# Kernel optimization log

Measured on AMD Instinct MI355X. Metric: run time of the kernel, lower is better.

Reference implementation:

```python
import jax, jax.numpy as jnp
import numpy as np

N_NODES = 100000
N_EDGES = 800000
D_R = 128   # node feature dim
D_H = 96    # edge message dim
D_OUT = 96  # output Linear out_features (bias removed per remove_bias)


def setup_inputs() -> dict:
    key = jax.random.key(0)
    k_r, k_h, k_nbr, k_w = jax.random.split(key, 4)
    r = jax.random.normal(k_r, (N_NODES, D_R), dtype=jnp.float32)
    h = jax.random.normal(k_h, (N_EDGES, D_H), dtype=jnp.float32)
    nbrs = jax.random.randint(k_nbr, (N_EDGES, 2), 0, N_NODES, dtype=jnp.int64)
    # Linear(D_R + D_H -> D_OUT, bias=False); torch Linear weight is [out, in]
    W_out = jax.random.normal(k_w, (D_OUT, D_R + D_H), dtype=jnp.float32) * (1.0 / np.sqrt(D_R + D_H))
    return {"r": r, "h": h, "nbrs": nbrs, "W_out": W_out}


def reference(r, h, nbrs, W_out):
    num_nodes = r.shape[0]
    # chemprop_msg_to_node: scatter-sum directed-edge messages onto destination node nbrs[:, 0]
    msg_to_node = jax.ops.segment_sum(h, nbrs[:, 0], num_segments=num_nodes)  # [N, D_H]
    cat_node = jnp.concatenate((r, msg_to_node), axis=1)                      # [N, D_R + D_H]
    new_node_feats = jax.nn.relu(cat_node @ W_out.T)                          # [N, D_OUT]
    return new_node_feats
```

## Files before the change

kernel.cpp:

```cpp
#include <hip/hip_runtime.h>
#include <hip/hip_bf16.h>

#define D_R 128
#define D_H 96
#define D_IN 224
#define D_OUT 96
#define WPAD 232
#define CAP 64

typedef __attribute__((ext_vector_type(8))) short short8;
typedef __attribute__((ext_vector_type(4))) float f32x4;

static __device__ inline unsigned short f2b(float x) {
    __hip_bfloat16 b = __float2bfloat16(x);
    unsigned short u;
    __builtin_memcpy(&u, &b, 2);
    return u;
}

__global__ __launch_bounds__(256) void zero_kernel(int* __restrict__ p, int n)
{
    int i = blockIdx.x * 256 + threadIdx.x;
    if (i < n) p[i] = 0;
}

__global__ __launch_bounds__(256) void convert_w_kernel(
    const float* __restrict__ W, unsigned short* __restrict__ W16, int n)
{
    int i = blockIdx.x * 256 + threadIdx.x;
    if (i < n) W16[i] = f2b(W[i]);
}

__global__ __launch_bounds__(256) void build_kernel(
    const int* __restrict__ nbrs, int* __restrict__ deg,
    int* __restrict__ bucket, int n_edges)
{
    int k = blockIdx.x * 256 + threadIdx.x;
    int e0 = 2 * k;
    if (e0 >= n_edges) return;
    if (e0 + 1 < n_edges) {
        int4 q = *reinterpret_cast<const int4*>(nbrs + 2 * e0);
        int p0 = atomicAdd(&deg[q.x], 1);
        if (p0 < CAP) bucket[(size_t)q.x * CAP + p0] = e0;
        int p1 = atomicAdd(&deg[q.z], 1);
        if (p1 < CAP) bucket[(size_t)q.z * CAP + p1] = e0 + 1;
    } else {
        int p0 = atomicAdd(&deg[nbrs[2 * e0]], 1);
        if (p0 < CAP) bucket[(size_t)nbrs[2 * e0] * CAP + p0] = e0;
    }
}

__global__ __launch_bounds__(256) void gather_kernel(
    const float* __restrict__ h, const int* __restrict__ deg_arr,
    const int* __restrict__ bucket, unsigned short* __restrict__ msg16,
    int n_nodes)
{
    int t = blockIdx.x * 256 + threadIdx.x;
    int node = t / 24;
    if (node >= n_nodes) return;
    int f4 = (t - node * 24) * 4;
    int deg = deg_arr[node]; if (deg > CAP) deg = CAP;
    const int* brow = bucket + (size_t)node * CAP;

    f32x4 a0 = (f32x4){0.f,0.f,0.f,0.f}, a1 = a0, a2 = a0, a3 = a0;
    int i = 0;
    for (; i + 4 <= deg; i += 4) {
        int4 e = *reinterpret_cast<const int4*>(brow + i);
        a0 += __builtin_nontemporal_load(
            reinterpret_cast<const f32x4*>(h + (size_t)e.x * D_H + f4));
        a1 += __builtin_nontemporal_load(
            reinterpret_cast<const f32x4*>(h + (size_t)e.y * D_H + f4));
        a2 += __builtin_nontemporal_load(
            reinterpret_cast<const f32x4*>(h + (size_t)e.z * D_H + f4));
        a3 += __builtin_nontemporal_load(
            reinterpret_cast<const f32x4*>(h + (size_t)e.w * D_H + f4));
    }
    for (; i < deg; ++i) {
        int e = brow[i];
        a0 += __builtin_nontemporal_load(
            reinterpret_cast<const f32x4*>(h + (size_t)e * D_H + f4));
    }
    f32x4 s = (a0 + a1) + (a2 + a3);
    ushort4 o;
    o.x = f2b(s.x); o.y = f2b(s.y); o.z = f2b(s.z); o.w = f2b(s.w);
    *reinterpret_cast<ushort4*>(msg16 + (size_t)node * D_H + f4) = o;
}

__global__ __launch_bounds__(256) void mfma_gemm_kernel(
    const float* __restrict__ r, const unsigned short* __restrict__ msg16,
    const unsigned short* __restrict__ W16, float* __restrict__ out, int n_nodes)
{
    __shared__ unsigned short Wl[D_OUT * WPAD];

    for (int c = threadIdx.x; c < D_OUT * (D_IN / 8); c += 256) {
        int j = c / 28, p = c - j * 28;
        *reinterpret_cast<short8*>(&Wl[j * WPAD + p * 8]) =
            *reinterpret_cast<const short8*>(&W16[j * D_IN + p * 8]);
    }
    __syncthreads();

    const int lane = threadIdx.x & 63;
    const int wv   = threadIdx.x >> 6;
    const int cl   = lane & 15;
    const int kch  = (lane >> 4) * 8;

    const int rowbase = blockIdx.x * 128 + wv * 32;

    f32x4 acc[2][6];
#pragma unroll
    for (int mf = 0; mf < 2; ++mf)
#pragma unroll
        for (int nf = 0; nf < 6; ++nf) acc[mf][nf] = (f32x4){0.f, 0.f, 0.f, 0.f};

    int arow0 = rowbase + cl;       if (arow0 >= n_nodes) arow0 = n_nodes - 1;
    int arow1 = rowbase + 16 + cl;  if (arow1 >= n_nodes) arow1 = n_nodes - 1;

    const float* rb[2] = { r + (size_t)arow0 * D_R + kch,
                           r + (size_t)arow1 * D_R + kch };
    const unsigned short* mb[2] = { msg16 + (size_t)arow0 * D_H + kch,
                                    msg16 + (size_t)arow1 * D_H + kch };

#pragma unroll
    for (int ks = 0; ks < 4; ++ks) {
        const int k0 = ks * 32;
        short8 a[2];
#pragma unroll
        for (int mf = 0; mf < 2; ++mf) {
            const f32x4 u = __builtin_nontemporal_load(
                reinterpret_cast<const f32x4*>(rb[mf] + k0));
            const f32x4 v = __builtin_nontemporal_load(
                reinterpret_cast<const f32x4*>(rb[mf] + k0 + 4));
            short8 tv;
            tv[0] = (short)f2b(u.x); tv[1] = (short)f2b(u.y);
            tv[2] = (short)f2b(u.z); tv[3] = (short)f2b(u.w);
            tv[4] = (short)f2b(v.x); tv[5] = (short)f2b(v.y);
            tv[6] = (short)f2b(v.z); tv[7] = (short)f2b(v.w);
            a[mf] = tv;
        }
#pragma unroll
        for (int nf = 0; nf < 6; ++nf) {
            const short8 b = *reinterpret_cast<const short8*>(
                &Wl[(nf * 16 + cl) * WPAD + k0 + kch]);
            acc[0][nf] = __builtin_amdgcn_mfma_f32_16x16x32_bf16(a[0], b, acc[0][nf], 0, 0, 0);
            acc[1][nf] = __builtin_amdgcn_mfma_f32_16x16x32_bf16(a[1], b, acc[1][nf], 0, 0, 0);
        }
    }

#pragma unroll
    for (int ks = 0; ks < 3; ++ks) {
        const int k0 = ks * 32;
        short8 a[2];
        a[0] = *reinterpret_cast<const short8*>(mb[0] + k0);
        a[1] = *reinterpret_cast<const short8*>(mb[1] + k0);
#pragma unroll
        for (int nf = 0; nf < 6; ++nf) {
            const short8 b = *reinterpret_cast<const short8*>(
                &Wl[(nf * 16 + cl) * WPAD + D_R + k0 + kch]);
            acc[0][nf] = __builtin_amdgcn_mfma_f32_16x16x32_bf16(a[0], b, acc[0][nf], 0, 0, 0);
            acc[1][nf] = __builtin_amdgcn_mfma_f32_16x16x32_bf16(a[1], b, acc[1][nf], 0, 0, 0);
        }
    }

    const int g4 = (lane >> 4) * 4;
#pragma unroll
    for (int mf = 0; mf < 2; ++mf) {
#pragma unroll
        for (int q = 0; q < 4; ++q) {
            const int row = rowbase + mf * 16 + g4 + q;
            if (row < n_nodes) {
                float* op = out + (size_t)row * D_OUT + cl;
#pragma unroll
                for (int nf = 0; nf < 6; ++nf)
                    __builtin_nontemporal_store(fmaxf(acc[mf][nf][q], 0.f), op + nf * 16);
            }
        }
    }
}

extern "C" void kernel_launch(void* const* d_in, const int* in_sizes, int n_in,
                              void* d_out, int out_size, void* d_ws, size_t ws_size,
                              hipStream_t stream) {
    const float* r    = (const float*)d_in[0];
    const float* h    = (const float*)d_in[1];
    const int*   nbrs = (const int*)d_in[2];
    const float* W    = (const float*)d_in[3];
    float*       out  = (float*)d_out;

    const int n_nodes = in_sizes[0] / D_R;
    const int n_edges = in_sizes[2] / 2;

    char* ws = (char*)d_ws;
    unsigned short* msg16 = (unsigned short*)ws;
    size_t off = (size_t)n_nodes * D_H * sizeof(unsigned short);
    int* deg    = (int*)(ws + off);  off += (size_t)n_nodes * sizeof(int);
    int* bucket = (int*)(ws + off);  off += (size_t)n_nodes * CAP * sizeof(int);
    unsigned short* W16 = (unsigned short*)(ws + off);

    const int pair_blocks = ((n_edges + 1) / 2 + 255) / 256;

    zero_kernel<<<(n_nodes + 255) / 256, 256, 0, stream>>>(deg, n_nodes);
    convert_w_kernel<<<(D_OUT * D_IN + 255) / 256, 256, 0, stream>>>(W, W16, D_OUT * D_IN);
    build_kernel<<<pair_blocks, 256, 0, stream>>>(nbrs, deg, bucket, n_edges);

    {
        long long total = (long long)n_nodes * 24;
        int blocks = (int)((total + 255) / 256);
        gather_kernel<<<blocks, 256, 0, stream>>>(h, deg, bucket, msg16, n_nodes);
    }
    {
        dim3 grid((n_nodes + 127) / 128);
        mfma_gemm_kernel<<<grid, 256, 0, stream>>>(r, msg16, W16, out, n_nodes);
    }
}
```

Baseline: 160.2 us.

## Fuse gather into GEMM kernel via LDS message tile and merge init kernels

```diff
diff --git a/kernel.cpp b/kernel.cpp
--- a/kernel.cpp
+++ b/kernel.cpp
@@ -5,8 +5,9 @@
 #define D_H 96
 #define D_IN 224
 #define D_OUT 96
-#define WPAD 232
 #define CAP 64
+#define MPAD 104
+#define NW 21504
 
 typedef __attribute__((ext_vector_type(8))) short short8;
 typedef __attribute__((ext_vector_type(4))) float f32x4;
@@ -18,17 +19,13 @@
     return u;
 }
 
-__global__ __launch_bounds__(256) void zero_kernel(int* __restrict__ p, int n)
+__global__ __launch_bounds__(256) void init_kernel(
+    int* __restrict__ deg, int n_nodes,
+    const float* __restrict__ W, unsigned short* __restrict__ W16)
 {
     int i = blockIdx.x * 256 + threadIdx.x;
-    if (i < n) p[i] = 0;
-}
-
-__global__ __launch_bounds__(256) void convert_w_kernel(
-    const float* __restrict__ W, unsigned short* __restrict__ W16, int n)
-{
-    int i = blockIdx.x * 256 + threadIdx.x;
-    if (i < n) W16[i] = f2b(W[i]);
+    if (i < n_nodes) deg[i] = 0;
+    if (i < NW) W16[i] = f2b(W[i]);
 }
 
 __global__ __launch_bounds__(256) void build_kernel(
@@ -45,57 +42,49 @@
         int p1 = atomicAdd(&deg[q.z], 1);
         if (p1 < CAP) bucket[(size_t)q.z * CAP + p1] = e0 + 1;
     } else {
-        int p0 = atomicAdd(&deg[nbrs[2 * e0]], 1);
-        if (p0 < CAP) bucket[(size_t)nbrs[2 * e0] * CAP + p0] = e0;
+        int d = nbrs[2 * e0];
+        int p0 = atomicAdd(&deg[d], 1);
+        if (p0 < CAP) bucket[(size_t)d * CAP + p0] = e0;
     }
 }
 
-__global__ __launch_bounds__(256) void gather_kernel(
-    const float* __restrict__ h, const int* __restrict__ deg_arr,
-    const int* __restrict__ bucket, unsigned short* __restrict__ msg16,
+__global__ __launch_bounds__(256) void fused_kernel(
+    const float* __restrict__ r, const float* __restrict__ h,
+    const int* __restrict__ deg_arr, const int* __restrict__ bucket,
+    const unsigned short* __restrict__ W16, float* __restrict__ out,
     int n_nodes)
 {
-    int t = blockIdx.x * 256 + threadIdx.x;
-    int node = t / 24;
-    if (node >= n_nodes) return;
-    int f4 = (t - node * 24) * 4;
-    int deg = deg_arr[node]; if (deg > CAP) deg = CAP;
-    const int* brow = bucket + (size_t)node * CAP;
+    __shared__ unsigned short msg_lds[128 * MPAD];
 
-    f32x4 a0 = (f32x4){0.f,0.f,0.f,0.f}, a1 = a0, a2 = a0, a3 = a0;
-    int i = 0;
-    for (; i + 4 <= deg; i += 4) {
-        int4 e = *reinterpret_cast<const int4*>(brow + i);
-        a0 += __builtin_nontemporal_load(
-            reinterpret_cast<const f32x4*>(h + (size_t)e.x * D_H + f4));
-        a1 += __builtin_nontemporal_load(
-            reinterpret_cast<const f32x4*>(h + (size_t)e.y * D_H + f4));
-        a2 += __builtin_nontemporal_load(
-            reinterpret_cast<const f32x4*>(h + (size_t)e.z * D_H + f4));
-        a3 += __builtin_nontemporal_load(
-            reinterpret_cast<const f32x4*>(h + (size_t)e.w * D_H + f4));
-    }
-    for (; i < deg; ++i) {
-        int e = brow[i];
-        a0 += __builtin_nontemporal_load(
-            reinterpret_cast<const f32x4*>(h + (size_t)e * D_H + f4));
-    }
-    f32x4 s = (a0 + a1) + (a2 + a3);
-    ushort4 o;
-    o.x = f2b(s.x); o.y = f2b(s.y); o.z = f2b(s.z); o.w = f2b(s.w);
-    *reinterpret_cast<ushort4*>(msg16 + (size_t)node * D_H + f4) = o;
-}
+    {
+        const int node_local = threadIdx.x >> 1;
+        const int half = threadIdx.x & 1;
+        const int node = blockIdx.x * 128 + node_local;
 
-__global__ __launch_bounds__(256) void mfma_gemm_kernel(
-    const float* __restrict__ r, const unsigned short* __restrict__ msg16,
-    const unsigned short* __restrict__ W16, float* __restrict__ out, int n_nodes)
-{
-    __shared__ unsigned short Wl[D_OUT * WPAD];
+        f32x4 g[12];
+#pragma unroll
+        for (int c = 0; c < 12; ++c) g[c] = (f32x4){0.f, 0.f, 0.f, 0.f};
 
-    for (int c = threadIdx.x; c < D_OUT * (D_IN / 8); c += 256) {
-        int j = c / 28, p = c - j * 28;
-        *reinterpret_cast<short8*>(&Wl[j * WPAD + p * 8]) =
-            *reinterpret_cast<const short8*>(&W16[j * D_IN + p * 8]);
+        if (node < n_nodes) {
+            int deg = deg_arr[node]; if (deg > CAP) deg = CAP;
+            const int* brow = bucket + (size_t)node * CAP;
+            for (int i = 0; i < deg; ++i) {
+                int e = brow[i];
+                const float* p = h + (size_t)e * D_H + half * 48;
+#pragma unroll
+                for (int c = 0; c < 12; ++c)
+                    g[c] += __builtin_nontemporal_load(
+                        reinterpret_cast<const f32x4*>(p + c * 4));
+            }
+        }
+        unsigned short* mrow = &msg_lds[node_local * MPAD + half * 48];
+#pragma unroll
+        for (int c = 0; c < 12; ++c) {
+            ushort4 o;
+            o.x = f2b(g[c].x); o.y = f2b(g[c].y);
+            o.z = f2b(g[c].z); o.w = f2b(g[c].w);
+            *reinterpret_cast<ushort4*>(mrow + c * 4) = o;
+        }
     }
     __syncthreads();
 
@@ -117,8 +106,8 @@
 
     const float* rb[2] = { r + (size_t)arow0 * D_R + kch,
                            r + (size_t)arow1 * D_R + kch };
-    const unsigned short* mb[2] = { msg16 + (size_t)arow0 * D_H + kch,
-                                    msg16 + (size_t)arow1 * D_H + kch };
+    const int lrow0 = wv * 32 + cl;
+    const int lrow1 = wv * 32 + 16 + cl;
 
 #pragma unroll
     for (int ks = 0; ks < 4; ++ks) {
@@ -140,7 +129,7 @@
 #pragma unroll
         for (int nf = 0; nf < 6; ++nf) {
             const short8 b = *reinterpret_cast<const short8*>(
-                &Wl[(nf * 16 + cl) * WPAD + k0 + kch]);
+                &W16[(nf * 16 + cl) * D_IN + k0 + kch]);
             acc[0][nf] = __builtin_amdgcn_mfma_f32_16x16x32_bf16(a[0], b, acc[0][nf], 0, 0, 0);
             acc[1][nf] = __builtin_amdgcn_mfma_f32_16x16x32_bf16(a[1], b, acc[1][nf], 0, 0, 0);
         }
@@ -150,12 +139,12 @@
     for (int ks = 0; ks < 3; ++ks) {
         const int k0 = ks * 32;
         short8 a[2];
-        a[0] = *reinterpret_cast<const short8*>(mb[0] + k0);
-        a[1] = *reinterpret_cast<const short8*>(mb[1] + k0);
+        a[0] = *reinterpret_cast<const short8*>(&msg_lds[lrow0 * MPAD + k0 + kch]);
+        a[1] = *reinterpret_cast<const short8*>(&msg_lds[lrow1 * MPAD + k0 + kch]);
 #pragma unroll
         for (int nf = 0; nf < 6; ++nf) {
             const short8 b = *reinterpret_cast<const short8*>(
-                &Wl[(nf * 16 + cl) * WPAD + D_R + k0 + kch]);
+                &W16[(nf * 16 + cl) * D_IN + D_R + k0 + kch]);
             acc[0][nf] = __builtin_amdgcn_mfma_f32_16x16x32_bf16(a[0], b, acc[0][nf], 0, 0, 0);
             acc[1][nf] = __builtin_amdgcn_mfma_f32_16x16x32_bf16(a[1], b, acc[1][nf], 0, 0, 0);
         }
@@ -190,25 +179,19 @@
     const int n_edges = in_sizes[2] / 2;
 
     char* ws = (char*)d_ws;
-    unsigned short* msg16 = (unsigned short*)ws;
-    size_t off = (size_t)n_nodes * D_H * sizeof(unsigned short);
-    int* deg    = (int*)(ws + off);  off += (size_t)n_nodes * sizeof(int);
+    int* deg    = (int*)ws;
+    size_t off = (size_t)n_nodes * sizeof(int);
     int* bucket = (int*)(ws + off);  off += (size_t)n_nodes * CAP * sizeof(int);
     unsigned short* W16 = (unsigned short*)(ws + off);
 
     const int pair_blocks = ((n_edges + 1) / 2 + 255) / 256;
+    const int init_blocks = (n_nodes > NW ? n_nodes : NW) / 256 + 1;
 
-    zero_kernel<<<(n_nodes + 255) / 256, 256, 0, stream>>>(deg, n_nodes);
-    convert_w_kernel<<<(D_OUT * D_IN + 255) / 256, 256, 0, stream>>>(W, W16, D_OUT * D_IN);
+    init_kernel<<<init_blocks, 256, 0, stream>>>(deg, n_nodes, W, W16);
     build_kernel<<<pair_blocks, 256, 0, stream>>>(nbrs, deg, bucket, n_edges);
 
     {
-        long long total = (long long)n_nodes * 24;
-        int blocks = (int)((total + 255) / 256);
-        gather_kernel<<<blocks, 256, 0, stream>>>(h, deg, bucket, msg16, n_nodes);
-    }
-    {
         dim3 grid((n_nodes + 127) / 128);
-        mfma_gemm_kernel<<<grid, 256, 0, stream>>>(r, msg16, W16, out, n_nodes);
+        fused_kernel<<<grid, 256, 0, stream>>>(r, h, deg, bucket, W16, out, n_nodes);
     }
 }
```

New measurement: 303.7 us. 1.9x slower.
